# Optimization experiments

Hardware: AMD Instinct MI355X
Metric: run time of the kernel (lower is better)

## Reference

```python
import jax, jax.numpy as jnp
import numpy as np

B, N, F = 4, 4096, 6
N_CENTROIDS, NSAMPLES, RADIUS = 1024, 64, 0.2


def fps(coords, n_c):
    # iterative farthest point sampling, vectorized over batch
    Bb, Nn, _ = coords.shape
    batch = jnp.arange(Bb)
    first = jnp.zeros((Bb,), jnp.int32)
    init_dist = jnp.full((Bb, Nn), 1e9, coords.dtype)

    def step(carry, _):
        dist, last = carry
        p = coords[batch, last]                      # (B,3) last chosen point
        d = jnp.sum((coords - p[:, None, :]) ** 2, -1)
        dist = jnp.minimum(dist, d)
        nxt = jnp.argmax(dist, -1).astype(jnp.int32)
        return (dist, nxt), nxt

    _, rest = jax.lax.scan(step, (init_dist, first), None, length=n_c - 1)
    return jnp.concatenate([first[None, :], rest], 0).T  # (B, n_c)


def ball_query(coords, centroids, radius, s):
    # coords (B,N,3), centroids (B,C,3) -> (B,C,S) neighbor indices
    Nn = coords.shape[1]
    d = jnp.sum((centroids[:, :, None, :] - coords[:, None, :, :]) ** 2, -1)  # (B,C,N)
    idx = jnp.where(d > radius * radius, Nn, jnp.arange(Nn))
    idx = jnp.sort(idx, axis=-1)[..., :s]
    first = idx[..., :1]                              # centroid itself always valid
    return jnp.where(idx == Nn, first, idx)


def tnet(h, w1, w2, w3, f1, f2):
    # h: (B, P, ch) -> (B, ch, ch) transform matrix (T-Net)
    ch = h.shape[-1]
    t = jax.nn.relu(h @ w1)
    t = jax.nn.relu(t @ w2)
    t = jax.nn.relu(t @ w3)
    t = t.max(axis=1)                                 # global max pool over points
    t = jax.nn.relu(t @ f1)
    return (t @ f2).reshape(-1, ch, ch) + jnp.eye(ch, dtype=h.dtype)


def setup_inputs() -> dict:
    key = jax.random.key(0)
    ks = jax.random.split(key, 20)
    sc = 0.02
    p = lambda k, shape: sc * jax.random.normal(k, shape, dtype=jnp.float32)
    return {
        'x': jax.random.normal(ks[0], (B, N, F), dtype=jnp.float32),
        'points': jax.random.uniform(ks[1], (B, N, 3), dtype=jnp.float32),
        # input T-Net (F x F)
        't1_w1': p(ks[2], (F, 64)), 't1_w2': p(ks[3], (64, 128)), 't1_w3': p(ks[4], (128, 256)),
        't1_f1': p(ks[5], (256, 128)), 't1_f2': p(ks[6], (128, F * F)),
        't2_w1': p(ks[7], (64, 64)), 't2_w2': p(ks[8], (64, 128)), 't2_w3': p(ks[9], (128, 256)),
        't2_f1': p(ks[10], (256, 128)), 't2_f2': p(ks[11], (128, 64 * 64)),
        # shared MLP
        'w1': p(ks[12], (F, 64)), 'w2': p(ks[13], (64, 128)), 'w3': p(ks[14], (128, 256)),
    }


def reference(x, points, t1_w1, t1_w2, t1_w3, t1_f1, t1_f2,
              t2_w1, t2_w2, t2_w3, t2_f1, t2_f2, w1, w2, w3):
    idx = fps(points, N_CENTROIDS)                                       # (B,C)
    centroids = jnp.take_along_axis(points, idx[..., None], axis=1)      # (B,C,3)
    gidx = ball_query(points, centroids, RADIUS, NSAMPLES)               # (B,C,S)
    gather = jax.vmap(lambda a, i: a[i])
    g_xyz = gather(points, gidx) - centroids[:, :, None, :]              # (B,C,S,3)
    g_feat = gather(x, gidx)                                             # (B,C,S,F)

    flat = g_feat.reshape(g_feat.shape[0], -1, g_feat.shape[-1])         # (B,C*S,F)
    inT = tnet(flat, t1_w1, t1_w2, t1_w3, t1_f1, t1_f2)                  # (B,F,F)
    h = jnp.einsum('bpc,bcd->bpd', flat, inT)
    h = jax.nn.relu(h @ w1)                                              # (B,C*S,64)
    feT = tnet(h, t2_w1, t2_w2, t2_w3, t2_f1, t2_f2)                     # (B,64,64)
    h = jnp.einsum('bpc,bcd->bpd', h, feT)
    h = jax.nn.relu(h @ w2)
    h = jax.nn.relu(h @ w3)                                              # (B,C*S,256)
    feats = h.reshape(h.shape[0], N_CENTROIDS, NSAMPLES, -1).max(axis=2) # (B,C,256)
    feats = feats.transpose(0, 2, 1)                                     # (B,256,C)
    return centroids, g_xyz.transpose(0, 3, 1, 2), feats, inT, feT
```

## Files before the change

### kernel.cpp

```cpp
#include <hip/hip_runtime.h>

#define Bb 4
#define Np 4096
#define Ff 6
#define NC 1024
#define NSAMP 64
#define NPTS (Bb*Np)
#define R2 ((float)(0.2*0.2))

static __host__ __device__ constexpr size_t alup(size_t x){ return (x + 255) & ~(size_t)255; }
static constexpr size_t OFF_GIDX = 0;
static constexpr size_t SZ_GIDX  = (size_t)Bb*NC*NSAMP*4;
static constexpr size_t OFF_MASK = alup(OFF_GIDX + SZ_GIDX);
static constexpr size_t SZ_MASK  = (size_t)Bb*Np*4;
static constexpr size_t OFF_T1   = OFF_MASK + SZ_MASK;
static constexpr size_t OFF_T2   = OFF_T1 + (size_t)Bb*256*4;
static constexpr size_t ZERO_BYTES = (OFF_T2 + (size_t)Bb*256*4) - OFF_MASK;
static constexpr size_t OFF_HW    = alup(OFF_T2 + (size_t)Bb*256*4);
static constexpr size_t OFF_FINAL = alup(OFF_HW + (size_t)64*NPTS*4);

__device__ __forceinline__ unsigned wave_red_umax(unsigned v)
{
#define DPP_STEP(ctrl) { unsigned t = (unsigned)__builtin_amdgcn_update_dpp((int)v, (int)v, ctrl, 0xF, 0xF, false); v = (t > v) ? t : v; }
    DPP_STEP(0x111)
    DPP_STEP(0x112)
    DPP_STEP(0x114)
    DPP_STEP(0x118)
    DPP_STEP(0x142)
    DPP_STEP(0x143)
#undef DPP_STEP
    return v;
}

template<int CTRL>
__device__ __forceinline__ double dpp_max_f64(double v)
{
    int lo = __double2loint(v), hi = __double2hiint(v);
    int tlo = __builtin_amdgcn_update_dpp(lo, lo, CTRL, 0xF, 0xF, false);
    int thi = __builtin_amdgcn_update_dpp(hi, hi, CTRL, 0xF, 0xF, false);
    return fmax(v, __hiloint2double(thi, tlo));
}

static constexpr int SMEM_BYTES = 84992;

__global__ __launch_bounds__(256) void mega_kernel(const float* __restrict__ points,
                                                   float* __restrict__ out_cent,
                                                   const float* __restrict__ x,
                                                   float* __restrict__ l3pre,
                                                   const float* __restrict__ t1w1,
                                                   const float* __restrict__ t1w2,
                                                   const float* __restrict__ t1w3)
{
    __shared__ __align__(16) char smem[SMEM_BYTES];

    if (blockIdx.x >= Bb) {
        int tb = blockIdx.x - Bb;
        int g0 = tb * 64;
        int t  = threadIdx.x;
        float* s_in  = (float*)(smem);
        float* s_w1  = (float*)(smem + 1536);
        float* s_a1  = (float*)(smem + 3072);
        float* s_wst = (float*)(smem + 19456);
        float* s_a2  = (float*)(smem + 52224);

        for (int i = t; i < 384; i += 256) {
            int pt = i / 6, c = i % 6;
            s_in[c * 64 + pt] = x[(size_t)(g0 + pt) * 6 + c];
        }
        for (int i = t; i < 384; i += 256)  s_w1[i]  = t1w1[i];
        for (int i = t; i < 8192; i += 256) s_wst[i] = t1w2[i];
        __syncthreads();

        int pt = t & 63;
        int grp = t >> 6;
        {
            int c0 = grp * 16;
            float a[16];
#pragma unroll
            for (int i = 0; i < 16; ++i) a[i] = 0.f;
#pragma unroll
            for (int k = 0; k < 6; ++k) {
                float av = s_in[k * 64 + pt];
#pragma unroll
                for (int i = 0; i < 16; ++i) a[i] += av * s_w1[k * 64 + c0 + i];
            }
#pragma unroll
            for (int i = 0; i < 16; ++i) s_a1[(c0 + i) * 64 + pt] = fmaxf(a[i], 0.f);
        }
        __syncthreads();
        {
            int cg = grp * 32;
            float a[32];
#pragma unroll
            for (int i = 0; i < 32; ++i) a[i] = 0.f;
#pragma unroll 2
            for (int k = 0; k < 64; ++k) {
                float av = s_a1[k * 64 + pt];
                const float4* w = (const float4*)&s_wst[k * 128 + cg];
#pragma unroll
                for (int q = 0; q < 8; ++q) {
                    float4 wv = w[q];
                    a[4*q+0] += av * wv.x; a[4*q+1] += av * wv.y;
                    a[4*q+2] += av * wv.z; a[4*q+3] += av * wv.w;
                }
            }
#pragma unroll
            for (int i = 0; i < 32; ++i) s_a2[(cg + i) * 64 + pt] = fmaxf(a[i], 0.f);
        }
        __syncthreads();
        for (int ch0 = 0; ch0 < 256; ch0 += 64) {
            for (int i = t; i < 8192; i += 256)
                s_wst[i] = t1w3[((size_t)(i >> 6) << 8) + ch0 + (i & 63)];
            __syncthreads();
            int cs = grp * 16;
            float a[16];
#pragma unroll
            for (int i = 0; i < 16; ++i) a[i] = 0.f;
#pragma unroll 2
            for (int k = 0; k < 128; ++k) {
                float av = s_a2[k * 64 + pt];
                const float4* w = (const float4*)&s_wst[k * 64 + cs];
#pragma unroll
                for (int q = 0; q < 4; ++q) {
                    float4 wv = w[q];
                    a[4*q+0] += av * wv.x; a[4*q+1] += av * wv.y;
                    a[4*q+2] += av * wv.z; a[4*q+3] += av * wv.w;
                }
            }
#pragma unroll
            for (int i = 0; i < 16; ++i)
                l3pre[(size_t)(ch0 + cs + i) * NPTS + g0 + pt] = a[i];
            __syncthreads();
        }
        return;
    }

    int b = blockIdx.x;
    const float* P = points + (size_t)b * Np * 3;
    int tid  = threadIdx.x;
    int lane = tid & 63;
    int wave = tid >> 6;

    float4* sc   = (float4*)(smem);
    double* swin = (double*)(smem + 65536);

    float px[16], py[16], pz[16], dist[16];
#pragma unroll
    for (int j = 0; j < 16; ++j) {
        int p = tid + (j << 8);
        float xx = P[p*3+0], yy = P[p*3+1], zz = P[p*3+2];
        px[j] = xx; py[j] = yy; pz[j] = zz;
        dist[j] = 1000000000.0f;
        sc[p] = make_float4(xx, yy, zz, 0.f);
    }
    __syncthreads();

    float cx = sc[0].x, cy = sc[0].y, cz = sc[0].z;
    if (tid == 0) {
        out_cent[((size_t)b*NC + 0)*3 + 0] = cx;
        out_cent[((size_t)b*NC + 0)*3 + 1] = cy;
        out_cent[((size_t)b*NC + 0)*3 + 2] = cz;
    }

    for (int s = 1; s < NC; ++s) {
        float m = -1.0f;
#pragma unroll
        for (int j = 0; j < 16; ++j) {
            float dx = __fsub_rn(px[j], cx);
            float dy = __fsub_rn(py[j], cy);
            float dz = __fsub_rn(pz[j], cz);
            float d  = __fadd_rn(__fadd_rn(__fmul_rn(dx,dx), __fmul_rn(dy,dy)), __fmul_rn(dz,dz));
            float nd = fminf(dist[j], d);
            dist[j] = nd;
            m = fmaxf(m, nd);
        }
        unsigned pj = 0u;
#pragma unroll
        for (int j = 15; j >= 0; --j)
            pj = (dist[j] == m) ? (unsigned)j : pj;
        unsigned lo = ~((unsigned)tid + (pj << 8));
        double key = __hiloint2double(__float_as_int(m), (int)lo);
        key = dpp_max_f64<0x111>(key);
        key = dpp_max_f64<0x112>(key);
        key = dpp_max_f64<0x114>(key);
        key = dpp_max_f64<0x118>(key);
        key = dpp_max_f64<0x142>(key);
        key = dpp_max_f64<0x143>(key);
        if (lane == 63) swin[(s & 1) * 4 + wave] = key;
        __syncthreads();

        const double2* sw = (const double2*)&swin[(s & 1) * 4];
        double2 p01 = sw[0], p23 = sw[1];
        double kk = fmax(fmax(p01.x, p01.y), fmax(p23.x, p23.y));
        int widx = ~__double2loint(kk);

        float4 c = sc[widx];
        cx = c.x; cy = c.y; cz = c.z;
        if (tid == 0) {
            out_cent[((size_t)b*NC + s)*3 + 0] = cx;
            out_cent[((size_t)b*NC + s)*3 + 1] = cy;
            out_cent[((size_t)b*NC + s)*3 + 2] = cz;
        }
    }
}

__global__ __launch_bounds__(256) void ballq_kernel(const float* __restrict__ points,
                                                    const float* __restrict__ cent,
                                                    int* __restrict__ gidx,
                                                    int* __restrict__ mask,
                                                    float* __restrict__ out_gxyz)
{
    int gtid = blockIdx.x * 256 + threadIdx.x;
    int wid  = gtid >> 6;
    int lane = threadIdx.x & 63;
    int b = wid >> 10, c = wid & 1023;
    const float* P = points + (size_t)b * Np * 3;
    float cx = cent[((size_t)b*NC + c)*3 + 0];
    float cy = cent[((size_t)b*NC + c)*3 + 1];
    float cz = cent[((size_t)b*NC + c)*3 + 2];

    __shared__ int sidx[4][NSAMP];
    int* my = sidx[threadIdx.x >> 6];

    int count = 0;
    for (int base = 0; base < Np; base += 64) {
        int p = base + lane;
        float dx = __fsub_rn(cx, P[p*3+0]);
        float dy = __fsub_rn(cy, P[p*3+1]);
        float dz = __fsub_rn(cz, P[p*3+2]);
        float d  = __fadd_rn(__fadd_rn(__fmul_rn(dx,dx), __fmul_rn(dy,dy)), __fmul_rn(dz,dz));
        bool inr = !(d > R2);
        unsigned long long mball = __ballot(inr);
        int before = __popcll(mball & ((1ull << lane) - 1ull));
        int pos = count + before;
        if (inr && pos < NSAMP) my[pos] = p;
        count += (int)__popcll(mball);
        if (count >= NSAMP) break;
    }
    __syncthreads();
    int total = count < NSAMP ? count : NSAMP;
    int first = my[0];
    int myi = (lane < total) ? my[lane] : first;
    gidx[(size_t)wid * NSAMP + lane] = myi;
    mask[(size_t)b * Np + myi] = 1;
    float qx = P[myi*3+0], qy = P[myi*3+1], qz = P[myi*3+2];
    out_gxyz[(((size_t)b*3 + 0)*NC + c)*NSAMP + lane] = __fsub_rn(qx, cx);
    out_gxyz[(((size_t)b*3 + 1)*NC + c)*NSAMP + lane] = __fsub_rn(qy, cy);
    out_gxyz[(((size_t)b*3 + 2)*NC + c)*NSAMP + lane] = __fsub_rn(qz, cz);
}

__global__ __launch_bounds__(256) void maxmask_kernel(const float* __restrict__ buf,
                                                      const int* __restrict__ mask,
                                                      float* __restrict__ tmax)
{
    int bid = blockIdx.x;
    int b = bid >> 8, ch = bid & 255;
    int tid = threadIdx.x;
    const float* row = buf + (size_t)ch * NPTS + (size_t)b * Np;
    const int* mk = mask + (size_t)b * Np;
    float m = 0.f;
#pragma unroll
    for (int i = 0; i < Np / 256; ++i) {
        int p = tid + i * 256;
        float v = row[p];
        if (mk[p]) m = fmaxf(m, fmaxf(v, 0.f));
    }
#pragma unroll
    for (int off = 1; off < 64; off <<= 1)
        m = fmaxf(m, __shfl_xor(m, off));
    __shared__ float red[4];
    if ((tid & 63) == 0) red[tid >> 6] = m;
    __syncthreads();
    if (tid == 0) {
        float r = fmaxf(fmaxf(red[0], red[1]), fmaxf(red[2], red[3]));
        tmax[(size_t)b * 256 + ch] = r;
    }
}

static constexpr int A_SMEM = 118784;

__global__ __launch_bounds__(256) void fused_t2_kernel(const float* __restrict__ x,
                                                       const float* __restrict__ t1max,
                                                       const float* __restrict__ f1,
                                                       const float* __restrict__ f2,
                                                       const float* __restrict__ w1,
                                                       const float* __restrict__ t2w1,
                                                       const float* __restrict__ t2w2,
                                                       const float* __restrict__ t2w3,
                                                       const int*   __restrict__ mask,
                                                       float* __restrict__ out_inT,
                                                       float* __restrict__ h_g,
                                                       unsigned* __restrict__ t2max)
{
    __shared__ __align__(16) char smem[A_SMEM];
    float* s_h  = (float*)(smem);
    float* s_b1 = (float*)(smem + 16384);
    float* s_b2 = (float*)(smem + 32768);
    float* s_wA = (float*)(smem + 65536);
    float* s_wB = (float*)(smem + 81920);
    float* tv   = (float*)(smem + 114688);
    float* u    = (float*)(smem + 115712);
    float* sT   = (float*)(smem + 116224);
    float* s_x  = (float*)(smem + 116480);

    int tb = blockIdx.x;
    int b  = tb >> 6;
    int g0 = tb * 64;
    int t  = threadIdx.x;
    int pt = t & 63;
    int grp = t >> 6;

    tv[t] = t1max[(size_t)b * 256 + t];
    for (int i = t; i < 384; i += 256) {
        int p = i / 6, c = i % 6;
        s_x[c * 64 + p] = x[(size_t)(g0 + p) * 6 + c];
    }
    for (int i = t; i < 4096; i += 256) s_wA[i] = t2w1[i];
    __syncthreads();
    if (t < 128) {
        float acc = 0.f;
        for (int k = 0; k < 256; ++k) acc += tv[k] * f1[(size_t)k*128 + t];
        u[t] = fmaxf(acc, 0.f);
    }
    __syncthreads();
    if (t < 36) {
        float acc = 0.f;
        for (int k = 0; k < 128; ++k) acc += u[k] * f2[(size_t)k*36 + t];
        if (t / 6 == t % 6) acc += 1.0f;
        sT[t] = acc;
        if ((tb & 63) == 0) out_inT[b*36 + t] = acc;
    }
    for (int i = t; i < 8192; i += 256) s_wB[i] = t2w2[i];
    __syncthreads();

    {
        float ttv[6];
#pragma unroll
        for (int o = 0; o < 6; ++o) {
            float acc = 0.f;
#pragma unroll
            for (int c = 0; c < 6; ++c) acc += s_x[c*64 + pt] * sT[c*6 + o];
            ttv[o] = acc;
        }
        int cg = grp * 16;
#pragma unroll
        for (int i = 0; i < 16; ++i) {
            float acc = 0.f;
#pragma unroll
            for (int o = 0; o < 6; ++o) acc += ttv[o] * w1[o*64 + cg + i];
            float hv = fmaxf(acc, 0.f);
            s_h[(cg + i) * 64 + pt] = hv;
            h_g[(size_t)(cg + i) * NPTS + g0 + pt] = hv;
        }
    }
    __syncthreads();

    {
        int cg = grp * 16;
        float a[16];
#pragma unroll
        for (int i = 0; i < 16; ++i) a[i] = 0.f;
#pragma unroll 2
        for (int k = 0; k < 64; ++k) {
            float av = s_h[k * 64 + pt];
            const float4* w = (const float4*)&s_wA[k * 64 + cg];
#pragma unroll
            for (int q = 0; q < 4; ++q) {
                float4 wv = w[q];
                a[4*q+0] += av * wv.x; a[4*q+1] += av * wv.y;
                a[4*q+2] += av * wv.z; a[4*q+3] += av * wv.w;
            }
        }
#pragma unroll
        for (int i = 0; i < 16; ++i) s_b1[(cg + i) * 64 + pt] = fmaxf(a[i], 0.f);
    }
    __syncthreads();

    {
        int cg = grp * 32;
        float a[32];
#pragma unroll
        for (int i = 0; i < 32; ++i) a[i] = 0.f;
#pragma unroll 2
        for (int k = 0; k < 64; ++k) {
            float av = s_b1[k * 64 + pt];
            const float4* w = (const float4*)&s_wB[k * 128 + cg];
#pragma unroll
            for (int q = 0; q < 8; ++q) {
                float4 wv = w[q];
                a[4*q+0] += av * wv.x; a[4*q+1] += av * wv.y;
                a[4*q+2] += av * wv.z; a[4*q+3] += av * wv.w;
            }
        }
#pragma unroll
        for (int i = 0; i < 32; ++i) s_b2[(cg + i) * 64 + pt] = fmaxf(a[i], 0.f);
    }
    __syncthreads();

    bool pres = mask[g0 + pt] != 0;
    for (int ch0 = 0; ch0 < 256; ch0 += 64) {
        for (int i = t; i < 8192; i += 256)
            s_wB[i] = t2w3[((size_t)(i >> 6) << 8) + ch0 + (i & 63)];
        __syncthreads();
        int cs = grp * 16;
        float a[16];
#pragma unroll
        for (int i = 0; i < 16; ++i) a[i] = 0.f;
#pragma unroll 2
        for (int k = 0; k < 128; ++k) {
            float av = s_b2[k * 64 + pt];
            const float4* w = (const float4*)&s_wB[k * 64 + cs];
#pragma unroll
            for (int q = 0; q < 4; ++q) {
                float4 wv = w[q];
                a[4*q+0] += av * wv.x; a[4*q+1] += av * wv.y;
                a[4*q+2] += av * wv.z; a[4*q+3] += av * wv.w;
            }
        }
#pragma unroll
        for (int i = 0; i < 16; ++i) {
            float v = pres ? fmaxf(a[i], 0.f) : 0.f;
            unsigned r = wave_red_umax(__float_as_uint(v));
            if ((t & 63) == 63)
                atomicMax(&t2max[(b << 8) + ch0 + cs + i], r);
        }
        __syncthreads();
    }
}

static constexpr int B_SMEM = 116224;

__global__ __launch_bounds__(256) void fused_tail_kernel(const unsigned* __restrict__ t2maxu,
                                                         const float* __restrict__ f1,
                                                         const float* __restrict__ f2,
                                                         const float* __restrict__ h_g,
                                                         const float* __restrict__ w2,
                                                         const float* __restrict__ w3,
                                                         float* __restrict__ out_feT,
                                                         float* __restrict__ final_g)
{
    __shared__ __align__(16) char smem[B_SMEM];
    float* s_h   = (float*)(smem);
    float* s_hf  = (float*)(smem + 16384);
    float* s_c1  = (float*)(smem + 32768);
    float* s_w   = (float*)(smem + 65536);
    float* s_feT = (float*)(smem + 98304);
    float* tv    = (float*)(smem + 114688);
    float* u     = (float*)(smem + 115712);

    int tb = blockIdx.x;
    int b  = tb >> 6;
    int g0 = tb * 64;
    int t  = threadIdx.x;
    int pt = t & 63;
    int grp = t >> 6;

    tv[t] = __uint_as_float(t2maxu[(size_t)b * 256 + t]);
    for (int i = t; i < 4096; i += 256)
        s_h[i] = h_g[(size_t)(i >> 6) * NPTS + g0 + (i & 63)];
    __syncthreads();
    if (t < 128) {
        float acc = 0.f;
        for (int k = 0; k < 256; ++k) acc += tv[k] * f1[(size_t)k*128 + t];
        u[t] = fmaxf(acc, 0.f);
    }
    for (int i = t; i < 8192; i += 256) s_w[i] = w2[i];
    __syncthreads();
    bool wrT = (tb & 63) == 0;
#pragma unroll
    for (int i = 0; i < 16; ++i) {
        int j = i * 256 + t;
        float acc = 0.f;
#pragma unroll 8
        for (int k = 0; k < 128; ++k) acc += u[k] * f2[(size_t)k*4096 + j];
        if ((j >> 6) == (j & 63)) acc += 1.0f;
        s_feT[j] = acc;
        if (wrT) out_feT[(size_t)b*4096 + j] = acc;
    }
    __syncthreads();

    {
        int cg = grp * 16;
        float a[16];
#pragma unroll
        for (int i = 0; i < 16; ++i) a[i] = 0.f;
#pragma unroll 2
        for (int k = 0; k < 64; ++k) {
            float av = s_h[k * 64 + pt];
            const float4* w = (const float4*)&s_feT[k * 64 + cg];
#pragma unroll
            for (int q = 0; q < 4; ++q) {
                float4 wv = w[q];
                a[4*q+0] += av * wv.x; a[4*q+1] += av * wv.y;
                a[4*q+2] += av * wv.z; a[4*q+3] += av * wv.w;
            }
        }
#pragma unroll
        for (int i = 0; i < 16; ++i) s_hf[(cg + i) * 64 + pt] = a[i];
    }
    __syncthreads();

    {
        int cg = grp * 32;
        float a[32];
#pragma unroll
        for (int i = 0; i < 32; ++i) a[i] = 0.f;
#pragma unroll 2
        for (int k = 0; k < 64; ++k) {
            float av = s_hf[k * 64 + pt];
            const float4* w = (const float4*)&s_w[k * 128 + cg];
#pragma unroll
            for (int q = 0; q < 8; ++q) {
                float4 wv = w[q];
                a[4*q+0] += av * wv.x; a[4*q+1] += av * wv.y;
                a[4*q+2] += av * wv.z; a[4*q+3] += av * wv.w;
            }
        }
#pragma unroll
        for (int i = 0; i < 32; ++i) s_c1[(cg + i) * 64 + pt] = fmaxf(a[i], 0.f);
    }
    __syncthreads();

    for (int ch0 = 0; ch0 < 256; ch0 += 64) {
        for (int i = t; i < 8192; i += 256)
            s_w[i] = w3[((size_t)(i >> 6) << 8) + ch0 + (i & 63)];
        __syncthreads();
        int cs = grp * 16;
        float a[16];
#pragma unroll
        for (int i = 0; i < 16; ++i) a[i] = 0.f;
#pragma unroll 2
        for (int k = 0; k < 128; ++k) {
            float av = s_c1[k * 64 + pt];
            const float4* w = (const float4*)&s_w[k * 64 + cs];
#pragma unroll
            for (int q = 0; q < 4; ++q) {
                float4 wv = w[q];
                a[4*q+0] += av * wv.x; a[4*q+1] += av * wv.y;
                a[4*q+2] += av * wv.z; a[4*q+3] += av * wv.w;
            }
        }
        float4* dst = (float4*)&final_g[(size_t)(g0 + pt) * 256 + ch0 + cs];
#pragma unroll
        for (int q = 0; q < 4; ++q)
            dst[q] = make_float4(fmaxf(a[4*q+0],0.f), fmaxf(a[4*q+1],0.f),
                                 fmaxf(a[4*q+2],0.f), fmaxf(a[4*q+3],0.f));
        __syncthreads();
    }
}

__global__ __launch_bounds__(256) void feats_kernel(const float* __restrict__ fin,
                                                    const int* __restrict__ gidx,
                                                    float* __restrict__ out)
{
    int bid = blockIdx.x;
    int b = bid >> 10, c = bid & 1023;
    int o = threadIdx.x;
    __shared__ int sid[NSAMP];
    if (o < NSAMP) sid[o] = gidx[(size_t)bid * NSAMP + o];
    __syncthreads();
    const float* fb = fin + (size_t)b * Np * 256;
    float m = -1e30f;
    for (int s = 0; s < NSAMP; ++s)
        m = fmaxf(m, fb[(size_t)sid[s] * 256 + o]);
    out[((size_t)b*256 + o)*NC + c] = m;
}

extern "C" void kernel_launch(void* const* d_in, const int* in_sizes, int n_in,
                              void* d_out, int out_size, void* d_ws, size_t ws_size,
                              hipStream_t stream)
{
    const float* x      = (const float*)d_in[0];
    const float* points = (const float*)d_in[1];
    const float* t1_w1  = (const float*)d_in[2];
    const float* t1_w2  = (const float*)d_in[3];
    const float* t1_w3  = (const float*)d_in[4];
    const float* t1_f1  = (const float*)d_in[5];
    const float* t1_f2  = (const float*)d_in[6];
    const float* t2_w1  = (const float*)d_in[7];
    const float* t2_w2  = (const float*)d_in[8];
    const float* t2_w3  = (const float*)d_in[9];
    const float* t2_f1  = (const float*)d_in[10];
    const float* t2_f2  = (const float*)d_in[11];
    const float* w1     = (const float*)d_in[12];
    const float* w2     = (const float*)d_in[13];
    const float* w3     = (const float*)d_in[14];

    float* out = (float*)d_out;
    float* out_cent  = out;
    float* out_gxyz  = out + 12288;
    float* out_feats = out + 798720;
    float* out_inT   = out + 1847296;
    float* out_feT   = out + 1847440;

    char* ws = (char*)d_ws;
    int*      gidx  = (int*)(ws + OFF_GIDX);
    int*      mask  = (int*)(ws + OFF_MASK);
    float*    t1max = (float*)(ws + OFF_T1);
    unsigned* t2max = (unsigned*)(ws + OFF_T2);
    float*    h_g   = (float*)(ws + OFF_HW);
    float*    fin   = (float*)(ws + OFF_FINAL);

    (void)hipMemsetAsync(ws + OFF_MASK, 0, ZERO_BYTES, stream);

    mega_kernel<<<Bb + 256, 256, 0, stream>>>(points, out_cent, x, fin, t1_w1, t1_w2, t1_w3);
    ballq_kernel<<<(Bb*NC)/4, 256, 0, stream>>>(points, out_cent, gidx, mask, out_gxyz);
    maxmask_kernel<<<Bb*256, 256, 0, stream>>>(fin, mask, t1max);
    fused_t2_kernel<<<256, 256, 0, stream>>>(x, t1max, t1_f1, t1_f2, w1,
                                             t2_w1, t2_w2, t2_w3, mask,
                                             out_inT, h_g, t2max);
    fused_tail_kernel<<<256, 256, 0, stream>>>(t2max, t2_f1, t2_f2, h_g, w2, w3,
                                               out_feT, fin);
    feats_kernel<<<Bb*NC, 256, 0, stream>>>(fin, gidx, out_feats);

    (void)in_sizes; (void)n_in; (void)out_size; (void)ws_size;
}
```

Before: 915.8 us.

## Pack FPS distance with index into f64 keys; hoist feature T-Net head into own kernel

The FPS loop now stores each point's running min distance together with its inverted index as a single double key. The per-thread argmax becomes four independent fmax chains, replacing the separate max and equality-scan pass. Separately, the feature T-Net head (f1/f2 matvecs producing feT) used to be recomputed redundantly in each of the 256 tail blocks. It now runs once in a small head2 kernel that writes feT to workspace, and the tail kernel just loads it. This costs an extra kernel launch and doubles the FPS register footprint for distances.

```diff
diff --git a/kernel.cpp b/kernel.cpp
--- a/kernel.cpp
+++ b/kernel.cpp
@@ -16,7 +16,8 @@
 static constexpr size_t OFF_T1   = OFF_MASK + SZ_MASK;
 static constexpr size_t OFF_T2   = OFF_T1 + (size_t)Bb*256*4;
 static constexpr size_t ZERO_BYTES = (OFF_T2 + (size_t)Bb*256*4) - OFF_MASK;
-static constexpr size_t OFF_HW    = alup(OFF_T2 + (size_t)Bb*256*4);
+static constexpr size_t OFF_FET  = alup(OFF_T2 + (size_t)Bb*256*4);
+static constexpr size_t OFF_HW    = alup(OFF_FET + (size_t)Bb*4096*4);
 static constexpr size_t OFF_FINAL = alup(OFF_HW + (size_t)64*NPTS*4);
 
 __device__ __forceinline__ unsigned wave_red_umax(unsigned v)
@@ -144,13 +145,14 @@
     float4* sc   = (float4*)(smem);
     double* swin = (double*)(smem + 65536);
 
-    float px[16], py[16], pz[16], dist[16];
+    float px[16], py[16], pz[16];
+    double dk[16];
 #pragma unroll
     for (int j = 0; j < 16; ++j) {
         int p = tid + (j << 8);
         float xx = P[p*3+0], yy = P[p*3+1], zz = P[p*3+2];
         px[j] = xx; py[j] = yy; pz[j] = zz;
-        dist[j] = 1000000000.0f;
+        dk[j] = __hiloint2double(__float_as_int(1000000000.0f), ~p);
         sc[p] = make_float4(xx, yy, zz, 0.f);
     }
     __syncthreads();
@@ -163,23 +165,22 @@
     }
 
     for (int s = 1; s < NC; ++s) {
-        float m = -1.0f;
+        double k0 = -1.0, k1 = -1.0, k2 = -1.0, k3 = -1.0;
 #pragma unroll
         for (int j = 0; j < 16; ++j) {
             float dx = __fsub_rn(px[j], cx);
             float dy = __fsub_rn(py[j], cy);
             float dz = __fsub_rn(pz[j], cz);
             float d  = __fadd_rn(__fadd_rn(__fmul_rn(dx,dx), __fmul_rn(dy,dy)), __fmul_rn(dz,dz));
-            float nd = fminf(dist[j], d);
-            dist[j] = nd;
-            m = fmaxf(m, nd);
-        }
-        unsigned pj = 0u;
-#pragma unroll
-        for (int j = 15; j >= 0; --j)
-            pj = (dist[j] == m) ? (unsigned)j : pj;
-        unsigned lo = ~((unsigned)tid + (pj << 8));
-        double key = __hiloint2double(__float_as_int(m), (int)lo);
+            float cur = __uint_as_float((unsigned)__double2hiint(dk[j]));
+            float nd  = fminf(cur, d);
+            dk[j] = __hiloint2double(__float_as_int(nd), __double2loint(dk[j]));
+            if      ((j & 3) == 0) k0 = fmax(k0, dk[j]);
+            else if ((j & 3) == 1) k1 = fmax(k1, dk[j]);
+            else if ((j & 3) == 2) k2 = fmax(k2, dk[j]);
+            else                   k3 = fmax(k3, dk[j]);
+        }
+        double key = fmax(fmax(k0, k1), fmax(k2, k3));
         key = dpp_max_f64<0x111>(key);
         key = dpp_max_f64<0x112>(key);
         key = dpp_max_f64<0x114>(key);
@@ -428,16 +429,37 @@
     }
 }
 
-static constexpr int B_SMEM = 116224;
-
-__global__ __launch_bounds__(256) void fused_tail_kernel(const unsigned* __restrict__ t2maxu,
-                                                         const float* __restrict__ f1,
-                                                         const float* __restrict__ f2,
-                                                         const float* __restrict__ h_g,
-                                                         const float* __restrict__ w2,
-                                                         const float* __restrict__ w3,
-                                                         float* __restrict__ out_feT,
-                                                         float* __restrict__ final_g)
+__global__ __launch_bounds__(256) void head2_kernel(const float* __restrict__ t2,
+                                                    const float* __restrict__ f1,
+                                                    const float* __restrict__ f2,
+                                                    float* __restrict__ outT, float* __restrict__ wsT)
+{
+    int b = blockIdx.x, t = threadIdx.x;
+    __shared__ float tv[256], u[128];
+    tv[t] = t2[(size_t)b*256 + t];
+    __syncthreads();
+    if (t < 128) {
+        float acc = 0.f;
+        for (int k = 0; k < 256; ++k) acc += tv[k] * f1[(size_t)k*128 + t];
+        u[t] = fmaxf(acc, 0.f);
+    }
+    __syncthreads();
+    int j = blockIdx.y * 256 + t;
+    float acc = 0.f;
+#pragma unroll 8
+    for (int k = 0; k < 128; ++k) acc += u[k] * f2[(size_t)k*4096 + j];
+    if (j / 64 == j % 64) acc += 1.0f;
+    outT[(size_t)b*4096 + j] = acc;
+    wsT[(size_t)b*4096 + j]  = acc;
+}
+
+static constexpr int B_SMEM = 114688;
+
+__global__ __launch_bounds__(256) void fused_hcf_kernel(const float* __restrict__ wsFeT,
+                                                        const float* __restrict__ h_g,
+                                                        const float* __restrict__ w2,
+                                                        const float* __restrict__ w3,
+                                                        float* __restrict__ final_g)
 {
     __shared__ __align__(16) char smem[B_SMEM];
     float* s_h   = (float*)(smem);
@@ -445,8 +467,6 @@
     float* s_c1  = (float*)(smem + 32768);
     float* s_w   = (float*)(smem + 65536);
     float* s_feT = (float*)(smem + 98304);
-    float* tv    = (float*)(smem + 114688);
-    float* u     = (float*)(smem + 115712);
 
     int tb = blockIdx.x;
     int b  = tb >> 6;
@@ -455,28 +475,11 @@
     int pt = t & 63;
     int grp = t >> 6;
 
-    tv[t] = __uint_as_float(t2maxu[(size_t)b * 256 + t]);
-    for (int i = t; i < 4096; i += 256)
-        s_h[i] = h_g[(size_t)(i >> 6) * NPTS + g0 + (i & 63)];
-    __syncthreads();
-    if (t < 128) {
-        float acc = 0.f;
-        for (int k = 0; k < 256; ++k) acc += tv[k] * f1[(size_t)k*128 + t];
-        u[t] = fmaxf(acc, 0.f);
+    for (int i = t; i < 4096; i += 256) {
+        s_h[i]   = h_g[(size_t)(i >> 6) * NPTS + g0 + (i & 63)];
+        s_feT[i] = wsFeT[(size_t)b * 4096 + i];
     }
     for (int i = t; i < 8192; i += 256) s_w[i] = w2[i];
-    __syncthreads();
-    bool wrT = (tb & 63) == 0;
-#pragma unroll
-    for (int i = 0; i < 16; ++i) {
-        int j = i * 256 + t;
-        float acc = 0.f;
-#pragma unroll 8
-        for (int k = 0; k < 128; ++k) acc += u[k] * f2[(size_t)k*4096 + j];
-        if ((j >> 6) == (j & 63)) acc += 1.0f;
-        s_feT[j] = acc;
-        if (wrT) out_feT[(size_t)b*4096 + j] = acc;
-    }
     __syncthreads();
 
     {
@@ -598,6 +601,7 @@
     int*      mask  = (int*)(ws + OFF_MASK);
     float*    t1max = (float*)(ws + OFF_T1);
     unsigned* t2max = (unsigned*)(ws + OFF_T2);
+    float*    wsFeT = (float*)(ws + OFF_FET);
     float*    h_g   = (float*)(ws + OFF_HW);
     float*    fin   = (float*)(ws + OFF_FINAL);
 
@@ -609,8 +613,8 @@
     fused_t2_kernel<<<256, 256, 0, stream>>>(x, t1max, t1_f1, t1_f2, w1,
                                              t2_w1, t2_w2, t2_w3, mask,
                                              out_inT, h_g, t2max);
-    fused_tail_kernel<<<256, 256, 0, stream>>>(t2max, t2_f1, t2_f2, h_g, w2, w3,
-                                               out_feT, fin);
+    head2_kernel<<<dim3(Bb,16), 256, 0, stream>>>((const float*)t2max, t2_f1, t2_f2, out_feT, wsFeT);
+    fused_hcf_kernel<<<256, 256, 0, stream>>>(wsFeT, h_g, w2, w3, fin);
     feats_kernel<<<Bb*NC, 256, 0, stream>>>(fin, gidx, out_feats);
 
     (void)in_sizes; (void)n_in; (void)out_size; (void)ws_size;
```

Measured after the change: 770.9 us. 1.19x faster.
